# Kernel optimization log

Hardware: AMD Instinct MI355X
Metric: run time of the kernel (lower is better)

## Reference

```python
import jax, jax.numpy as jnp
import numpy as np

WEIGHT_BIT = 8
ACT_BIT = 8
EPS = 1e-8

def ste_round(v):
    # straight-through estimator round (matches torch ste_round in QAT)
    return v + jax.lax.stop_gradient(jnp.round(v) - v)

def setup_inputs() -> dict:
    key = jax.random.key(0)
    k1, k2, k3, k4 = jax.random.split(key, 4)
    B, D_IN, D_OUT = 8192, 4096, 4096
    x = jax.random.normal(k1, (B, D_IN), dtype=jnp.float32)
    act_scaling_factor = jax.random.uniform(k2, (1,), dtype=jnp.float32, minval=0.01, maxval=0.05)
    W = jax.random.normal(k3, (D_OUT, D_IN), dtype=jnp.float32) * 0.02
    b = jax.random.normal(k4, (D_OUT,), dtype=jnp.float32) * 0.02
    return {"x": x, "act_scaling_factor": act_scaling_factor, "W": W, "b": b}

def reference(x, act_scaling_factor, W, b):
    n_w = 2 ** (WEIGHT_BIT - 1) - 1  # 127
    # ---- QuantLinear: symmetric per-channel weight quantization ----
    w_absmax = jnp.maximum(jnp.abs(W.min(axis=1)), jnp.abs(W.max(axis=1)))  # [out]
    fc_sf = jnp.maximum(w_absmax, EPS) / n_w  # weight scaling factor, [out]
    w_int = jnp.clip(ste_round(W / fc_sf[:, None]), -n_w - 1, n_w)
    bias_sf = fc_sf * act_scaling_factor  # [out] (act_sf is scalar-shaped [1])
    b_int = ste_round(b / bias_sf)
    x_int = x / act_scaling_factor
    out = (jnp.matmul(x_int, w_int.T) + b_int) * bias_sf  # [B, out]
    # ---- ReLU ----
    out = jax.nn.relu(out)
    # ---- QuantAct, asymmetric per-tensor requantization ----
    levels = 2 ** ACT_BIT - 1  # 255
    x_min = jnp.minimum(out.min(), 0.0)
    x_max = jnp.maximum(out.max(), 0.0)
    act_sf_new = jnp.maximum(x_max - x_min, EPS) / levels  # scalar
    zp = jnp.round(-x_min / act_sf_new)
    x_q = jnp.clip(ste_round(out / act_sf_new) + zp, 0.0, float(levels))
    x_out = (x_q - zp) * act_sf_new
    return (x_out, fc_sf, jnp.reshape(act_sf_new, (1,)))
```

## Files before the change

### kernel.cpp

```cpp
#include <hip/hip_runtime.h>
#include <hip/hip_bf16.h>
#include <stdint.h>

#define B_DIM 8192
#define IN_DIM 4096
#define OUT_DIM 4096
#define NT (IN_DIM / 64)

typedef __attribute__((ext_vector_type(8))) short s16x8;
typedef __attribute__((ext_vector_type(4))) float f32x4;

__device__ __forceinline__ unsigned short f2bf_rn(float f) {
    unsigned int u = __float_as_uint(f);
    u = (u + 0x7FFFu + ((u >> 16) & 1u)) >> 16;
    return (unsigned short)u;
}

__device__ __forceinline__ void async16(unsigned short* l, const unsigned short* g) {
    __builtin_amdgcn_global_load_lds(
        (const __attribute__((address_space(1))) void*)g,
        (__attribute__((address_space(3))) void*)l, 16, 0, 0);
}

__global__ __launch_bounds__(256) void prep(
    const float* __restrict__ W, const float* __restrict__ b,
    const float* __restrict__ act_sf, const float* __restrict__ x,
    unsigned short* __restrict__ wq, unsigned short* __restrict__ xq,
    float* __restrict__ fc_sf_out, float* __restrict__ bb,
    float* __restrict__ gmax)
{
    __shared__ float red[4];
    int t = threadIdx.x;
    if (blockIdx.x < OUT_DIM) {
        int o = blockIdx.x;
        const float4* Wr = (const float4*)(W + (size_t)o * IN_DIM);
        float4 v[4];
        float amax = 0.f;
#pragma unroll
        for (int j = 0; j < 4; ++j) {
            v[j] = Wr[t + j * 256];
            amax = fmaxf(amax, fmaxf(fmaxf(fabsf(v[j].x), fabsf(v[j].y)),
                                     fmaxf(fabsf(v[j].z), fabsf(v[j].w))));
        }
#pragma unroll
        for (int off = 32; off > 0; off >>= 1)
            amax = fmaxf(amax, __shfl_down(amax, off, 64));
        if ((t & 63) == 0) red[t >> 6] = amax;
        __syncthreads();
        float wmax = fmaxf(fmaxf(red[0], red[1]), fmaxf(red[2], red[3]));
        float sf = fmaxf(wmax, 1e-8f) / 127.0f;

        unsigned short* wr = wq + (size_t)o * IN_DIM;
#pragma unroll
        for (int j = 0; j < 4; ++j) {
            ushort4 q;
            q.x = f2bf_rn(fminf(fmaxf(rintf(v[j].x / sf), -128.f), 127.f));
            q.y = f2bf_rn(fminf(fmaxf(rintf(v[j].y / sf), -128.f), 127.f));
            q.z = f2bf_rn(fminf(fmaxf(rintf(v[j].z / sf), -128.f), 127.f));
            q.w = f2bf_rn(fminf(fmaxf(rintf(v[j].w / sf), -128.f), 127.f));
            ((ushort4*)wr)[t + j * 256] = q;
        }
        if (t == 0) {
            fc_sf_out[o] = sf;
            float bsf = sf * act_sf[0];
            float bi = rintf(b[o] / bsf);
            bb[o] = bi * bsf;
            if (o == 0) gmax[0] = 0.f;
        }
    } else {
        size_t i = ((size_t)(blockIdx.x - OUT_DIM) * 256 + t) * 8;
#pragma unroll
        for (int j = 0; j < 2; ++j) {
            float4 v = *(const float4*)(x + i + j * 4);
            ushort4 q;
            q.x = f2bf_rn(v.x); q.y = f2bf_rn(v.y);
            q.z = f2bf_rn(v.z); q.w = f2bf_rn(v.w);
            *(ushort4*)(xq + i + j * 4) = q;
        }
    }
}

template <bool CB16>
__global__ __launch_bounds__(512) void gemm_bt(
    const unsigned short* __restrict__ A, const unsigned short* __restrict__ Bw,
    const float* __restrict__ fc_sf, const float* __restrict__ bb,
    void* __restrict__ Cout, float* __restrict__ gmax)
{
    __shared__ __align__(16) unsigned char smem[131072];
    unsigned short* lds = (unsigned short*)smem;
    float* stage = (float*)smem;
    float* redm  = (float*)(smem + 131040);

    int t = threadIdx.x;
    int bid = ((blockIdx.x & 7) << 6) | (blockIdx.x >> 3);
    int bm = bid >> 4, bn = bid & 15;
    int m0 = bm << 8, n0 = bn << 8;

    int w = t >> 6, lane = t & 63;
    int wm = w & 1, wn = w >> 1;
    int quad = lane >> 4, l16 = lane & 15;
    int swz = l16 & 7;

    int co0 = (quad ^ swz) << 3;
    int co1 = ((quad + 4) ^ swz) << 3;
    int aOff = ((wm << 4) + l16) << 6;
    int bOff = 32768 + (((wn << 4) + l16) << 6);

    int r0 = t >> 3;
    int cs = ((t & 7) ^ (r0 & 7)) << 3;
    const unsigned short* gA = A + (size_t)(m0 + r0) * IN_DIM + cs;
    const unsigned short* gB = Bw + (size_t)(n0 + r0) * IN_DIM + cs;
    unsigned short* ldsA = lds + t * 8;
    unsigned short* ldsB = lds + 32768 + t * 8;

    auto stageA = [&](int u, int hf) {
        if (u < NT) {
            const unsigned short* s = gA + (size_t)(hf * 128) * IN_DIM + u * 64;
            unsigned short* d = ldsA + ((u & 1) << 14) + (hf << 13);
            async16(d, s);
            async16(d + 4096, s + (size_t)64 * IN_DIM);
        }
    };
    auto stageB = [&](int u, int hf) {
        if (u < NT) {
            const unsigned short* s = gB + (size_t)(hf * 128) * IN_DIM + u * 64;
            unsigned short* d = ldsB + ((u & 1) << 14) + (hf << 13);
            async16(d, s);
            async16(d + 4096, s + (size_t)64 * IN_DIM);
        }
    };

    f32x4 acc[8][4];
#pragma unroll
    for (int mi = 0; mi < 8; ++mi)
#pragma unroll
        for (int nj = 0; nj < 4; ++nj)
            acc[mi][nj] = (f32x4){0.f, 0.f, 0.f, 0.f};

    s16x8 aLo[4][2], aHi[4][2], bF[2][2];

    stageA(0, 0); stageA(0, 1); stageB(0, 0); stageB(0, 1);
    stageA(1, 0); stageA(1, 1); stageB(1, 0);
    asm volatile("s_waitcnt vmcnt(6)" ::: "memory");
    __builtin_amdgcn_s_barrier();

    for (int kt = 0; kt < NT; ++kt) {
        int bufo = (kt & 1) << 14;
        const unsigned short* la = lds + bufo + aOff;
        const unsigned short* lb = lds + bufo + bOff;

#pragma unroll
        for (int mi = 0; mi < 4; ++mi) {
            aLo[mi][0] = *(const s16x8*)(la + mi * 2048 + co0);
            aLo[mi][1] = *(const s16x8*)(la + mi * 2048 + co1);
        }
#pragma unroll
        for (int nj = 0; nj < 2; ++nj) {
            bF[nj][0] = *(const s16x8*)(lb + nj * 4096 + co0);
            bF[nj][1] = *(const s16x8*)(lb + nj * 4096 + co1);
        }
        stageB(kt + 1, 1);
        __builtin_amdgcn_s_barrier();
        asm volatile("s_waitcnt lgkmcnt(0)" ::: "memory");
        __builtin_amdgcn_sched_barrier(0);
        __builtin_amdgcn_s_setprio(1);
#pragma unroll
        for (int mi = 0; mi < 4; ++mi)
#pragma unroll
            for (int nj = 0; nj < 2; ++nj) {
                acc[mi][nj] = __builtin_amdgcn_mfma_f32_16x16x32_bf16(aLo[mi][0], bF[nj][0], acc[mi][nj], 0, 0, 0);
                acc[mi][nj] = __builtin_amdgcn_mfma_f32_16x16x32_bf16(aLo[mi][1], bF[nj][1], acc[mi][nj], 0, 0, 0);
            }
        __builtin_amdgcn_s_setprio(0);
        __builtin_amdgcn_s_barrier();

#pragma unroll
        for (int mi = 0; mi < 4; ++mi) {
            aHi[mi][0] = *(const s16x8*)(la + 8192 + mi * 2048 + co0);
            aHi[mi][1] = *(const s16x8*)(la + 8192 + mi * 2048 + co1);
        }
        stageA(kt + 2, 0);
        __builtin_amdgcn_s_barrier();
        asm volatile("s_waitcnt lgkmcnt(0)" ::: "memory");
        __builtin_amdgcn_sched_barrier(0);
        __builtin_amdgcn_s_setprio(1);
#pragma unroll
        for (int mi = 0; mi < 4; ++mi)
#pragma unroll
            for (int nj = 0; nj < 2; ++nj) {
                acc[4 + mi][nj] = __builtin_amdgcn_mfma_f32_16x16x32_bf16(aHi[mi][0], bF[nj][0], acc[4 + mi][nj], 0, 0, 0);
                acc[4 + mi][nj] = __builtin_amdgcn_mfma_f32_16x16x32_bf16(aHi[mi][1], bF[nj][1], acc[4 + mi][nj], 0, 0, 0);
            }
        __builtin_amdgcn_s_setprio(0);
        __builtin_amdgcn_s_barrier();

#pragma unroll
        for (int nj = 0; nj < 2; ++nj) {
            bF[nj][0] = *(const s16x8*)(lb + 8192 + nj * 4096 + co0);
            bF[nj][1] = *(const s16x8*)(lb + 8192 + nj * 4096 + co1);
        }
        stageA(kt + 2, 1);
        __builtin_amdgcn_s_barrier();
        asm volatile("s_waitcnt lgkmcnt(0)" ::: "memory");
        __builtin_amdgcn_sched_barrier(0);
        __builtin_amdgcn_s_setprio(1);
#pragma unroll
        for (int mi = 0; mi < 4; ++mi)
#pragma unroll
            for (int nj = 0; nj < 2; ++nj) {
                acc[4 + mi][2 + nj] = __builtin_amdgcn_mfma_f32_16x16x32_bf16(aHi[mi][0], bF[nj][0], acc[4 + mi][2 + nj], 0, 0, 0);
                acc[4 + mi][2 + nj] = __builtin_amdgcn_mfma_f32_16x16x32_bf16(aHi[mi][1], bF[nj][1], acc[4 + mi][2 + nj], 0, 0, 0);
            }
        __builtin_amdgcn_s_setprio(0);
        __builtin_amdgcn_s_barrier();

        stageB(kt + 2, 0);
        __builtin_amdgcn_s_barrier();
        __builtin_amdgcn_s_setprio(1);
#pragma unroll
        for (int mi = 0; mi < 4; ++mi)
#pragma unroll
            for (int nj = 0; nj < 2; ++nj) {
                acc[mi][2 + nj] = __builtin_amdgcn_mfma_f32_16x16x32_bf16(aLo[mi][0], bF[nj][0], acc[mi][2 + nj], 0, 0, 0);
                acc[mi][2 + nj] = __builtin_amdgcn_mfma_f32_16x16x32_bf16(aLo[mi][1], bF[nj][1], acc[mi][2 + nj], 0, 0, 0);
            }
        __builtin_amdgcn_s_setprio(0);
        if (kt + 2 < NT)
            asm volatile("s_waitcnt vmcnt(6)" ::: "memory");
        else if (kt + 2 == NT)
            asm volatile("s_waitcnt vmcnt(0)" ::: "memory");
        __builtin_amdgcn_s_barrier();
    }

    float sc[4], bv[4];
#pragma unroll
    for (int nj = 0; nj < 4; ++nj) {
        int col = n0 + (((nj << 2) + wn) << 4) + l16;
        sc[nj] = fc_sf[col];
        bv[nj] = bb[col];
    }
    float tmax = 0.f;
#pragma unroll
    for (int mi = 0; mi < 8; ++mi)
#pragma unroll
        for (int nj = 0; nj < 4; ++nj)
#pragma unroll
            for (int r = 0; r < 4; ++r) {
                float vv = fmaxf(acc[mi][nj][r] * sc[nj] + bv[nj], 0.f);
                acc[mi][nj][r] = vv;
                tmax = fmaxf(tmax, vv);
            }
#pragma unroll
    for (int off = 32; off > 0; off >>= 1)
        tmax = fmaxf(tmax, __shfl_down(tmax, off, 64));
    if (lane == 0) redm[w] = tmax;

#pragma unroll
    for (int ph = 0; ph < 4; ++ph) {
        __syncthreads();
#pragma unroll
        for (int ml = 0; ml < 2; ++ml) {
            int lrow = (((ml << 1) + wm) << 4) + (quad << 2);
#pragma unroll
            for (int nj = 0; nj < 4; ++nj) {
                int col = (((nj << 2) + wn) << 4) + l16;
#pragma unroll
                for (int r = 0; r < 4; ++r)
                    stage[(lrow + r) * 260 + col] = acc[ph * 2 + ml][nj][r];
            }
        }
        __syncthreads();
        int row = t >> 3, ch = t & 7;
        const float* src = stage + row * 260 + ch * 32;
        size_t gbase = (size_t)(m0 + ph * 64 + row) * OUT_DIM + n0 + ch * 32;
        if (CB16) {
            unsigned short* dst = (unsigned short*)Cout + gbase;
#pragma unroll
            for (int j = 0; j < 4; ++j) {
                float4 v0 = *(const float4*)(src + j * 8);
                float4 v1 = *(const float4*)(src + j * 8 + 4);
                s16x8 q;
                q[0] = (short)f2bf_rn(v0.x); q[1] = (short)f2bf_rn(v0.y);
                q[2] = (short)f2bf_rn(v0.z); q[3] = (short)f2bf_rn(v0.w);
                q[4] = (short)f2bf_rn(v1.x); q[5] = (short)f2bf_rn(v1.y);
                q[6] = (short)f2bf_rn(v1.z); q[7] = (short)f2bf_rn(v1.w);
                *(s16x8*)(dst + j * 8) = q;
            }
        } else {
            float* dst = (float*)Cout + gbase;
#pragma unroll
            for (int j = 0; j < 8; ++j)
                *(float4*)(dst + j * 4) = *(const float4*)(src + j * 4);
        }
    }
    if (t == 0) {
        float bmax = redm[0];
#pragma unroll
        for (int i = 1; i < 8; ++i) bmax = fmaxf(bmax, redm[i]);
        atomicMax((int*)gmax, __float_as_int(bmax));
    }
}

template <bool CB16>
__global__ __launch_bounds__(256) void requant(const void* __restrict__ Cin,
    float* __restrict__ out, const float* __restrict__ gmax,
    float* __restrict__ sf_out)
{
    float sf = fmaxf(gmax[0], 1e-8f) / 255.0f;
    size_t i = ((size_t)blockIdx.x * 256 + threadIdx.x) * 16;
    if (CB16) {
        const unsigned short* cq = (const unsigned short*)Cin + i;
#pragma unroll
        for (int j = 0; j < 4; ++j) {
            ushort4 q = *(const ushort4*)(cq + j * 4);
            float4 v;
            v.x = __uint_as_float((unsigned)q.x << 16);
            v.y = __uint_as_float((unsigned)q.y << 16);
            v.z = __uint_as_float((unsigned)q.z << 16);
            v.w = __uint_as_float((unsigned)q.w << 16);
            v.x = fminf(rintf(v.x / sf), 255.f) * sf;
            v.y = fminf(rintf(v.y / sf), 255.f) * sf;
            v.z = fminf(rintf(v.z / sf), 255.f) * sf;
            v.w = fminf(rintf(v.w / sf), 255.f) * sf;
            *(float4*)(out + i + j * 4) = v;
        }
    } else {
        float* C = out;
#pragma unroll
        for (int j = 0; j < 4; ++j) {
            float4 v = *(const float4*)(C + i + j * 4);
            v.x = fminf(rintf(v.x / sf), 255.f) * sf;
            v.y = fminf(rintf(v.y / sf), 255.f) * sf;
            v.z = fminf(rintf(v.z / sf), 255.f) * sf;
            v.w = fminf(rintf(v.w / sf), 255.f) * sf;
            *(float4*)(C + i + j * 4) = v;
        }
    }
    if (i == 0) sf_out[0] = sf;
}

extern "C" void kernel_launch(void* const* d_in, const int* in_sizes, int n_in,
                              void* d_out, int out_size, void* d_ws, size_t ws_size,
                              hipStream_t stream)
{
    const float* x      = (const float*)d_in[0];
    const float* act_sf = (const float*)d_in[1];
    const float* W      = (const float*)d_in[2];
    const float* b      = (const float*)d_in[3];

    float* out        = (float*)d_out;
    float* fc_sf_out  = out + (size_t)B_DIM * OUT_DIM;
    float* act_sf_out = fc_sf_out + OUT_DIM;

    char* ws = (char*)d_ws;
    float* bb   = (float*)ws;
    float* gmax = (float*)(ws + 16384);
    unsigned short* xq = (unsigned short*)(ws + 32768);
    unsigned short* wq = xq + (size_t)B_DIM * IN_DIM;
    unsigned short* cq = wq + (size_t)OUT_DIM * IN_DIM;

    size_t need = 32768 + ((size_t)B_DIM * IN_DIM + (size_t)OUT_DIM * IN_DIM
                           + (size_t)B_DIM * OUT_DIM) * 2;

    prep<<<OUT_DIM + (B_DIM * IN_DIM) / 2048, 256, 0, stream>>>(
        W, b, act_sf, x, wq, xq, fc_sf_out, bb, gmax);

    int gemm_grid = (B_DIM / 256) * (OUT_DIM / 256);
    int rq_grid = (B_DIM * OUT_DIM) / 4096;
    if (ws_size >= need) {
        gemm_bt<true><<<gemm_grid, 512, 0, stream>>>(
            xq, wq, fc_sf_out, bb, (void*)cq, gmax);
        requant<true><<<rq_grid, 256, 0, stream>>>(
            (const void*)cq, out, gmax, act_sf_out);
    } else {
        gemm_bt<false><<<gemm_grid, 512, 0, stream>>>(
            xq, wq, fc_sf_out, bb, (void*)out, gmax);
        requant<false><<<rq_grid, 256, 0, stream>>>(
            (const void*)out, out, gmax, act_sf_out);
    }
}
```

Before: 528.8 us.

## Restructure GEMM main loop into 8-phase ping-pong register pipeline

Rewrites the bf16 MFMA main loop as an 8-phase schedule over two k-tiles. It double-buffers A and B fragments in registers (a0/a1, b0/b1), so LDS reads for the next quadrant overlap the MFMAs of the current one. Waits are partial (lgkmcnt/vmcnt counts) instead of full drains, and out-of-range stage calls are clamped to reload valid tiles rather than skipped, which keeps vmcnt accounting uniform. This aims to hide LDS and global latency behind compute, at the cost of more registers, redundant tail loads and fragile hand-tuned wait counts.

Result: no change. 527.3 us (-0.3%).

```diff
diff --git a/kernel.cpp b/kernel.cpp
--- a/kernel.cpp
+++ b/kernel.cpp
@@ -113,22 +113,42 @@
     unsigned short* ldsA = lds + t * 8;
     unsigned short* ldsB = lds + 32768 + t * 8;
 
-    auto stageA = [&](int u, int hf) {
-        if (u < NT) {
-            const unsigned short* s = gA + (size_t)(hf * 128) * IN_DIM + u * 64;
-            unsigned short* d = ldsA + ((u & 1) << 14) + (hf << 13);
-            async16(d, s);
-            async16(d + 4096, s + (size_t)64 * IN_DIM);
-        }
-    };
-    auto stageB = [&](int u, int hf) {
-        if (u < NT) {
-            const unsigned short* s = gB + (size_t)(hf * 128) * IN_DIM + u * 64;
-            unsigned short* d = ldsB + ((u & 1) << 14) + (hf << 13);
-            async16(d, s);
-            async16(d + 4096, s + (size_t)64 * IN_DIM);
-        }
-    };
+#define STA(u, hf) { int uu_ = (u) < NT ? (u) : ((u) - 2 < NT ? (u) - 2 : (u) - 4); \
+    const unsigned short* s_ = gA + (size_t)((hf) * 128) * IN_DIM + uu_ * 64;       \
+    unsigned short* d_ = ldsA + ((uu_ & 1) << 14) + ((hf) << 13);                   \
+    async16(d_, s_); async16(d_ + 4096, s_ + (size_t)64 * IN_DIM); }
+#define STB(u, hf) { int uu_ = (u) < NT ? (u) : ((u) - 2 < NT ? (u) - 2 : (u) - 4); \
+    const unsigned short* s_ = gB + (size_t)((hf) * 128) * IN_DIM + uu_ * 64;       \
+    unsigned short* d_ = ldsB + ((uu_ & 1) << 14) + ((hf) << 13);                   \
+    async16(d_, s_); async16(d_ + 4096, s_ + (size_t)64 * IN_DIM); }
+
+#define RD_A(dst, base) _Pragma("unroll") \
+    for (int mi_ = 0; mi_ < 4; ++mi_) { \
+        dst[mi_][0] = *(const s16x8*)((base) + mi_ * 2048 + co0); \
+        dst[mi_][1] = *(const s16x8*)((base) + mi_ * 2048 + co1); }
+#define RD_B(dst, base) _Pragma("unroll") \
+    for (int nj_ = 0; nj_ < 2; ++nj_) { \
+        dst[nj_][0] = *(const s16x8*)((base) + nj_ * 4096 + co0); \
+        dst[nj_][1] = *(const s16x8*)((base) + nj_ * 4096 + co1); }
+
+#define QUAD(MB, NB, AF, BF) _Pragma("unroll") \
+    for (int mi_ = 0; mi_ < 4; ++mi_) { _Pragma("unroll") \
+        for (int nj_ = 0; nj_ < 2; ++nj_) { \
+            acc[(MB)+mi_][(NB)+nj_] = __builtin_amdgcn_mfma_f32_16x16x32_bf16( \
+                AF[mi_][0], BF[nj_][0], acc[(MB)+mi_][(NB)+nj_], 0, 0, 0); \
+            acc[(MB)+mi_][(NB)+nj_] = __builtin_amdgcn_mfma_f32_16x16x32_bf16( \
+                AF[mi_][1], BF[nj_][1], acc[(MB)+mi_][(NB)+nj_], 0, 0, 0); } }
+
+#define PHASE(RD, NCNT, ST, MM) \
+    RD; \
+    asm volatile("s_waitcnt lgkmcnt(" #NCNT ")" ::: "memory"); \
+    __builtin_amdgcn_sched_barrier(0); \
+    asm volatile("s_waitcnt vmcnt(10)" ::: "memory"); \
+    __builtin_amdgcn_s_barrier(); \
+    ST; \
+    __builtin_amdgcn_s_setprio(1); \
+    MM; \
+    __builtin_amdgcn_s_setprio(0);
 
     f32x4 acc[8][4];
 #pragma unroll
@@ -137,100 +157,42 @@
         for (int nj = 0; nj < 4; ++nj)
             acc[mi][nj] = (f32x4){0.f, 0.f, 0.f, 0.f};
 
-    s16x8 aLo[4][2], aHi[4][2], bF[2][2];
-
-    stageA(0, 0); stageA(0, 1); stageB(0, 0); stageB(0, 1);
-    stageA(1, 0); stageA(1, 1); stageB(1, 0);
-    asm volatile("s_waitcnt vmcnt(6)" ::: "memory");
+    s16x8 a0[4][2], a1[4][2], b0[2][2], b1[2][2];
+
+    STA(0, 0); STB(0, 0); STB(0, 1); STA(0, 1); STA(1, 0); STB(1, 0); STB(1, 1);
+    asm volatile("s_waitcnt vmcnt(12)" ::: "memory");
     __builtin_amdgcn_s_barrier();
-
-    for (int kt = 0; kt < NT; ++kt) {
-        int bufo = (kt & 1) << 14;
-        const unsigned short* la = lds + bufo + aOff;
-        const unsigned short* lb = lds + bufo + bOff;
-
-#pragma unroll
-        for (int mi = 0; mi < 4; ++mi) {
-            aLo[mi][0] = *(const s16x8*)(la + mi * 2048 + co0);
-            aLo[mi][1] = *(const s16x8*)(la + mi * 2048 + co1);
-        }
-#pragma unroll
-        for (int nj = 0; nj < 2; ++nj) {
-            bF[nj][0] = *(const s16x8*)(lb + nj * 4096 + co0);
-            bF[nj][1] = *(const s16x8*)(lb + nj * 4096 + co1);
-        }
-        stageB(kt + 1, 1);
-        __builtin_amdgcn_s_barrier();
-        asm volatile("s_waitcnt lgkmcnt(0)" ::: "memory");
-        __builtin_amdgcn_sched_barrier(0);
-        __builtin_amdgcn_s_setprio(1);
-#pragma unroll
-        for (int mi = 0; mi < 4; ++mi)
-#pragma unroll
-            for (int nj = 0; nj < 2; ++nj) {
-                acc[mi][nj] = __builtin_amdgcn_mfma_f32_16x16x32_bf16(aLo[mi][0], bF[nj][0], acc[mi][nj], 0, 0, 0);
-                acc[mi][nj] = __builtin_amdgcn_mfma_f32_16x16x32_bf16(aLo[mi][1], bF[nj][1], acc[mi][nj], 0, 0, 0);
-            }
-        __builtin_amdgcn_s_setprio(0);
-        __builtin_amdgcn_s_barrier();
-
-#pragma unroll
-        for (int mi = 0; mi < 4; ++mi) {
-            aHi[mi][0] = *(const s16x8*)(la + 8192 + mi * 2048 + co0);
-            aHi[mi][1] = *(const s16x8*)(la + 8192 + mi * 2048 + co1);
-        }
-        stageA(kt + 2, 0);
-        __builtin_amdgcn_s_barrier();
-        asm volatile("s_waitcnt lgkmcnt(0)" ::: "memory");
-        __builtin_amdgcn_sched_barrier(0);
-        __builtin_amdgcn_s_setprio(1);
-#pragma unroll
-        for (int mi = 0; mi < 4; ++mi)
-#pragma unroll
-            for (int nj = 0; nj < 2; ++nj) {
-                acc[4 + mi][nj] = __builtin_amdgcn_mfma_f32_16x16x32_bf16(aHi[mi][0], bF[nj][0], acc[4 + mi][nj], 0, 0, 0);
-                acc[4 + mi][nj] = __builtin_amdgcn_mfma_f32_16x16x32_bf16(aHi[mi][1], bF[nj][1], acc[4 + mi][nj], 0, 0, 0);
-            }
-        __builtin_amdgcn_s_setprio(0);
-        __builtin_amdgcn_s_barrier();
-
-#pragma unroll
-        for (int nj = 0; nj < 2; ++nj) {
-            bF[nj][0] = *(const s16x8*)(lb + 8192 + nj * 4096 + co0);
-            bF[nj][1] = *(const s16x8*)(lb + 8192 + nj * 4096 + co1);
-        }
-        stageA(kt + 2, 1);
-        __builtin_amdgcn_s_barrier();
-        asm volatile("s_waitcnt lgkmcnt(0)" ::: "memory");
-        __builtin_amdgcn_sched_barrier(0);
-        __builtin_amdgcn_s_setprio(1);
-#pragma unroll
-        for (int mi = 0; mi < 4; ++mi)
-#pragma unroll
-            for (int nj = 0; nj < 2; ++nj) {
-                acc[4 + mi][2 + nj] = __builtin_amdgcn_mfma_f32_16x16x32_bf16(aHi[mi][0], bF[nj][0], acc[4 + mi][2 + nj], 0, 0, 0);
-                acc[4 + mi][2 + nj] = __builtin_amdgcn_mfma_f32_16x16x32_bf16(aHi[mi][1], bF[nj][1], acc[4 + mi][2 + nj], 0, 0, 0);
-            }
-        __builtin_amdgcn_s_setprio(0);
-        __builtin_amdgcn_s_barrier();
-
-        stageB(kt + 2, 0);
-        __builtin_amdgcn_s_barrier();
-        __builtin_amdgcn_s_setprio(1);
-#pragma unroll
-        for (int mi = 0; mi < 4; ++mi)
-#pragma unroll
-            for (int nj = 0; nj < 2; ++nj) {
-                acc[mi][2 + nj] = __builtin_amdgcn_mfma_f32_16x16x32_bf16(aLo[mi][0], bF[nj][0], acc[mi][2 + nj], 0, 0, 0);
-                acc[mi][2 + nj] = __builtin_amdgcn_mfma_f32_16x16x32_bf16(aLo[mi][1], bF[nj][1], acc[mi][2 + nj], 0, 0, 0);
-            }
-        __builtin_amdgcn_s_setprio(0);
-        if (kt + 2 < NT)
-            asm volatile("s_waitcnt vmcnt(6)" ::: "memory");
-        else if (kt + 2 == NT)
-            asm volatile("s_waitcnt vmcnt(0)" ::: "memory");
-        __builtin_amdgcn_s_barrier();
-    }
+    RD_A(a0, lds + aOff);
+    asm volatile("s_waitcnt lgkmcnt(8)" ::: "memory");
+    __builtin_amdgcn_sched_barrier(0);
+    asm volatile("s_waitcnt vmcnt(10)" ::: "memory");
+    __builtin_amdgcn_s_barrier();
+    STA(1, 1);
+    RD_B(b0, lds + bOff);
+    asm volatile("s_waitcnt lgkmcnt(4)" ::: "memory");
+    __builtin_amdgcn_sched_barrier(0);
+    asm volatile("s_waitcnt vmcnt(10)" ::: "memory");
+    __builtin_amdgcn_s_barrier();
+    STA(2, 0);
+
+    for (int T = 0; T < NT; T += 2) {
+        const unsigned short* laT  = lds + ((T & 1) << 14) + aOff;
+        const unsigned short* lbT  = lds + ((T & 1) << 14) + bOff;
+        const unsigned short* laT1 = lds + (((T + 1) & 1) << 14) + aOff;
+        const unsigned short* lbT1 = lds + (((T + 1) & 1) << 14) + bOff;
+
+        PHASE( RD_B(b1, lbT + 8192),  4, STB(T + 2, 0), QUAD(0, 0, a0, b0) );
+        PHASE( RD_A(a1, laT + 8192),  8, STB(T + 2, 1), QUAD(0, 2, a0, b1) );
+        PHASE( RD_A(a0, laT1),        8, STA(T + 2, 1), QUAD(4, 0, a1, b0) );
+        PHASE( RD_B(b0, lbT1),        4, STA(T + 3, 0), QUAD(4, 2, a1, b1) );
+        PHASE( RD_B(b1, lbT1 + 8192), 4, STB(T + 3, 0), QUAD(0, 0, a0, b0) );
+        PHASE( RD_A(a1, laT1 + 8192), 8, STB(T + 3, 1), QUAD(0, 2, a0, b1) );
+        PHASE( RD_A(a0, laT),         8, STA(T + 3, 1), QUAD(4, 0, a1, b0) );
+        PHASE( RD_B(b0, lbT),         4, STA(T + 4, 0), QUAD(4, 2, a1, b1) );
+    }
+
+    asm volatile("s_waitcnt vmcnt(0) lgkmcnt(0)" ::: "memory");
+    __syncthreads();
 
     float sc[4], bv[4];
 #pragma unroll
@@ -299,6 +261,12 @@
         for (int i = 1; i < 8; ++i) bmax = fmaxf(bmax, redm[i]);
         atomicMax((int*)gmax, __float_as_int(bmax));
     }
+#undef STA
+#undef STB
+#undef RD_A
+#undef RD_B
+#undef QUAD
+#undef PHASE
 }
 
 template <bool CB16>
```
